# Optimization experiments

Hardware: AMD Instinct MI355X
Metric: run time of the kernel (lower is better)

Reference implementation:

```python
import jax, jax.numpy as jnp
import numpy as np

N, E, D, R = 50000, 1200000, 128, 6  # nodes, edges, channels (dim_in==dim_out), relations
NEG_SLOPE = 0.2


def setup_inputs() -> dict:
    key = jax.random.key(0)
    ks = jax.random.split(key, 7)
    x = jax.random.normal(ks[0], (N, D), jnp.float32)
    edge_index = jax.random.randint(ks[1], (2, E), 0, N)
    edge_type = jax.random.randint(ks[2], (E,), 0, R)
    # RGATConv params (heads=1): weight [R, D, D], q/k [D, 1], bias [D]
    weight = jax.random.normal(ks[3], (R, D, D), jnp.float32) * 0.05
    q = jax.random.normal(ks[4], (D, 1), jnp.float32) * 0.05
    k = jax.random.normal(ks[5], (D, 1), jnp.float32) * 0.05
    bias = jnp.zeros((D,), jnp.float32)
    return dict(x=x, edge_index=edge_index, edge_type=edge_type,
                weight=weight, q=q, k=k, bias=bias)


def segment_softmax(logits, seg, num_segments):
    m = jax.ops.segment_max(logits, seg, num_segments=num_segments)
    m = jnp.where(jnp.isfinite(m), m, 0.0)  # empty segments -> 0
    e = jnp.exp(logits - m[seg])
    s = jax.ops.segment_sum(e, seg, num_segments=num_segments)
    return e / (s[seg] + 1e-16)


def reference(x, edge_index, edge_type, weight, q, k, bias):
    src, dst = edge_index[0], edge_index[1]  # message flows src(j) -> dst(i)
    # per-node, per-relation transform W_r x_n : [R, N, D]
    hx = jnp.einsum('nd,rdo->rno', x, weight)
    # attention projections (heads=1): scalar per node per relation
    nq = jnp.einsum('rno,o->rn', hx, q[:, 0])  # q_i component
    nk = jnp.einsum('rno,o->rn', hx, k[:, 0])  # k_j component
    # additive self-attention, across-relation softmax over incoming edges
    logits = jax.nn.leaky_relu(nq[edge_type, dst] + nk[edge_type, src], NEG_SLOPE)
    alpha = segment_softmax(logits, dst, N)  # [E]
    # message = alpha * (W_r x_j), scatter-add into dst; dropout inactive (eval)
    msg = alpha[:, None] * hx[edge_type, src]  # [E, D]
    agg = jax.ops.segment_sum(msg, dst, num_segments=N) + bias
    out = agg + x  # residual add in GATLayer.forward
    return out, alpha[:, None]  # attention weights: [E, heads=1]
```

## Files before the change

kernel.cpp:

```cpp
#include <hip/hip_runtime.h>
#include <hip/hip_bf16.h>
#include <cstdint>

#define NN 50000
#define NE 1200000
#define DD 128
#define RR 6
#define NEG 0.2f
#define NB 391
#define CAP 4096
#define TILE 4096
#define GEMMB 782

typedef __hip_bfloat16 bf16;
typedef __attribute__((ext_vector_type(8))) short short8;
typedef __attribute__((ext_vector_type(4))) float f32x4;

__device__ __forceinline__ float bflo(unsigned u) { return __uint_as_float(u << 16); }
__device__ __forceinline__ float bfhi(unsigned u) { return __uint_as_float(u & 0xFFFF0000u); }
__device__ __forceinline__ ushort f2b(float v) {
  unsigned b = __float_as_uint(v);
  return (ushort)((b + 0x7FFFu + ((b >> 16) & 1u)) >> 16);
}

__global__ __launch_bounds__(256) void k_prep(const float* __restrict__ W,
    const float* __restrict__ qv, const float* __restrict__ kv,
    ushort* __restrict__ wp, ushort* __restrict__ wp7, int* __restrict__ bcur) {
  int t = blockIdx.x * 256 + threadIdx.x;
  if (t < NB) bcur[t] = 0;
  if (t < RR * 8 * 4 * 64) {
    int lane = t & 63;
    int ks = (t >> 6) & 3;
    int cf = (t >> 8) & 7;
    int r = t >> 11;
    int col = cf * 16 + (lane & 15);
    int k0 = ks * 32 + (lane >> 4) * 8;
    ushort* dst = wp + (size_t)t * 8;
    #pragma unroll
    for (int e = 0; e < 8; ++e)
      dst[e] = f2b(W[((size_t)r * DD + (k0 + e)) * DD + col]);
  } else if (t < RR * 8 * 4 * 64 + 256) {
    int idx = t - RR * 8 * 4 * 64;
    int lane = idx & 63, ks = idx >> 6;
    int col = lane & 15;
    int k0 = ks * 32 + (lane >> 4) * 8;
    ushort* dst = wp7 + (size_t)idx * 8;
    #pragma unroll
    for (int e = 0; e < 8; ++e) {
      float v = 0.f;
      if (col < 12) {
        int r = col < 6 ? col : col - 6;
        const float* vv = col < 6 ? qv : kv;
        const float* row = W + ((size_t)r * DD + (k0 + e)) * DD;
        for (int o = 0; o < DD; ++o) v += row[o] * vv[o];
      }
      dst[e] = f2b(v);
    }
  }
}

__global__ __launch_bounds__(256) void k_gemm(const float* __restrict__ x,
    const ushort* __restrict__ wp, const ushort* __restrict__ wp7,
    ushort* __restrict__ hx, float* __restrict__ nq, float* __restrict__ nk) {
  __shared__ ushort tile[64][136];
  int tid = threadIdx.x;
  int w = tid >> 6, l = tid & 63;
  int wrow = w & 1, wcol = w >> 1;
  int row0 = blockIdx.x * 64;
  int rbase = row0 + wrow * 32;
  int lr = l & 15, lg = l >> 4;

  short8 af[2][4];
  #pragma unroll
  for (int rf = 0; rf < 2; ++rf) {
    int row = rbase + rf * 16 + lr;
    row = row < NN ? row : NN - 1;
    const float* src = x + (size_t)row * DD + lg * 8;
    #pragma unroll
    for (int ks = 0; ks < 4; ++ks) {
      float4 u0 = *reinterpret_cast<const float4*>(src + ks * 32);
      float4 u1 = *reinterpret_cast<const float4*>(src + ks * 32 + 4);
      short8 a;
      a[0] = (short)f2b(u0.x); a[1] = (short)f2b(u0.y);
      a[2] = (short)f2b(u0.z); a[3] = (short)f2b(u0.w);
      a[4] = (short)f2b(u1.x); a[5] = (short)f2b(u1.y);
      a[6] = (short)f2b(u1.z); a[7] = (short)f2b(u1.w);
      af[rf][ks] = a;
    }
  }

  if (wcol == 0) {
    f32x4 aq0 = {0.f, 0.f, 0.f, 0.f}, aq1 = {0.f, 0.f, 0.f, 0.f};
    #pragma unroll
    for (int ks = 0; ks < 4; ++ks) {
      short8 b = *reinterpret_cast<const short8*>(wp7 + (size_t)(ks * 64 + l) * 8);
      aq0 = __builtin_amdgcn_mfma_f32_16x16x32_bf16(af[0][ks], b, aq0, 0, 0, 0);
      aq1 = __builtin_amdgcn_mfma_f32_16x16x32_bf16(af[1][ks], b, aq1, 0, 0, 0);
    }
    if (lr < 12) {
      float* pl = (lr < 6 ? nq + (size_t)lr * NN : nk + (size_t)(lr - 6) * NN);
      #pragma unroll
      for (int rf = 0; rf < 2; ++rf) {
        int rowb = rbase + rf * 16 + lg * 4;
        f32x4 v = rf ? aq1 : aq0;
        if (rowb + 3 < NN) {
          float4 o4 = make_float4(v[0], v[1], v[2], v[3]);
          *reinterpret_cast<float4*>(pl + rowb) = o4;
        } else {
          #pragma unroll
          for (int j = 0; j < 4; ++j) if (rowb + j < NN) pl[rowb + j] = v[j];
        }
      }
    }
  }

  for (int r = 0; r < RR; ++r) {
    #pragma unroll
    for (int cfl = 0; cfl < 4; ++cfl) {
      int cfg = wcol * 4 + cfl;
      const ushort* bp = wp + (((size_t)(r * 8 + cfg) * 4) * 64 + l) * 8;
      short8 b0 = *reinterpret_cast<const short8*>(bp);
      short8 b1 = *reinterpret_cast<const short8*>(bp + 512);
      short8 b2 = *reinterpret_cast<const short8*>(bp + 1024);
      short8 b3 = *reinterpret_cast<const short8*>(bp + 1536);
      f32x4 acc0 = {0.f, 0.f, 0.f, 0.f};
      f32x4 acc1 = {0.f, 0.f, 0.f, 0.f};
      acc0 = __builtin_amdgcn_mfma_f32_16x16x32_bf16(af[0][0], b0, acc0, 0, 0, 0);
      acc1 = __builtin_amdgcn_mfma_f32_16x16x32_bf16(af[1][0], b0, acc1, 0, 0, 0);
      acc0 = __builtin_amdgcn_mfma_f32_16x16x32_bf16(af[0][1], b1, acc0, 0, 0, 0);
      acc1 = __builtin_amdgcn_mfma_f32_16x16x32_bf16(af[1][1], b1, acc1, 0, 0, 0);
      acc0 = __builtin_amdgcn_mfma_f32_16x16x32_bf16(af[0][2], b2, acc0, 0, 0, 0);
      acc1 = __builtin_amdgcn_mfma_f32_16x16x32_bf16(af[1][2], b2, acc1, 0, 0, 0);
      acc0 = __builtin_amdgcn_mfma_f32_16x16x32_bf16(af[0][3], b3, acc0, 0, 0, 0);
      acc1 = __builtin_amdgcn_mfma_f32_16x16x32_bf16(af[1][3], b3, acc1, 0, 0, 0);

      int col = cfg * 16 + lr;
      #pragma unroll
      for (int rf = 0; rf < 2; ++rf) {
        int rowrel = wrow * 32 + rf * 16 + lg * 4;
        f32x4 ac = rf ? acc1 : acc0;
        #pragma unroll
        for (int j = 0; j < 4; ++j)
          tile[rowrel + j][col] = f2b(ac[j]);
      }
    }
    __syncthreads();
    #pragma unroll
    for (int it = 0; it < 4; ++it) {
      int rowrel = (tid >> 4) + it * 16;
      int grow = row0 + rowrel;
      uint4 v = *reinterpret_cast<const uint4*>(&tile[rowrel][(tid & 15) * 8]);
      if (grow < NN)
        *reinterpret_cast<uint4*>(hx + ((size_t)r * NN + grow) * DD + (tid & 15) * 8) = v;
    }
    __syncthreads();
  }
}

__global__ __launch_bounds__(256) void k_bscatter(const int* __restrict__ ei,
    const int* __restrict__ et, int* __restrict__ bcur,
    unsigned* __restrict__ bedge) {
  __shared__ unsigned sval[TILE];
  __shared__ unsigned short sbkt[TILE];
  __shared__ int lh[NB], lbase[NB], lcur[NB];
  int tid = threadIdx.x;
  int e0 = blockIdx.x * TILE;
  int lim = NE - e0; if (lim > TILE) lim = TILE;
  for (int i = tid; i < NB; i += 256) lh[i] = 0;
  __syncthreads();
  for (int i = tid; i < lim; i += 256) {
    int e = e0 + i;
    int s = ei[e], d = ei[NE + e], r = et[e];
    unsigned rowid = (unsigned)(r * NN + s);
    sval[i] = (rowid << 3) | (unsigned)r | ((unsigned)(d & 127) << 22);
    sbkt[i] = (unsigned short)(d >> 7);
    atomicAdd(&lh[d >> 7], 1);
  }
  __syncthreads();
  for (int i = tid; i < NB; i += 256) {
    int c = lh[i];
    lbase[i] = c ? atomicAdd(&bcur[i], c) : 0;
    lcur[i] = 0;
  }
  __syncthreads();
  for (int i = tid; i < lim; i += 256) {
    int b = sbkt[i];
    int pos = b * CAP + lbase[b] + atomicAdd(&lcur[b], 1);
    bedge[pos] = sval[i];
  }
}

__global__ __launch_bounds__(256) void k_bfinal(const unsigned* __restrict__ bedge,
    const int* __restrict__ bcur,
    const float* __restrict__ nq, const float* __restrict__ nk,
    int* __restrict__ deg, int* __restrict__ offs, unsigned* __restrict__ rec) {
  __shared__ int lh[128], sc_s[128], lcur[128];
  int b = blockIdx.x, tid = threadIdx.x;
  int base = b * CAP, cnt = bcur[b];
  if (tid < 128) lh[tid] = 0;
  __syncthreads();
  for (int i = tid; i < cnt; i += 256)
    atomicAdd(&lh[(bedge[base + i] >> 22) & 127], 1);
  __syncthreads();
  int v = 0;
  if (tid < 128) { v = lh[tid]; sc_s[tid] = v; }
  __syncthreads();
  for (int off = 1; off < 128; off <<= 1) {
    int u = (tid < 128 && tid >= off) ? sc_s[tid - off] : 0;
    __syncthreads();
    if (tid < 128) sc_s[tid] += u;
    __syncthreads();
  }
  if (tid < 128) {
    int excl = sc_s[tid] - v;
    int n = (b << 7) + tid;
    if (n < NN) { deg[n] = v; offs[n] = base + excl; }
    lcur[tid] = base + excl;
  }
  __syncthreads();
  for (int i = tid; i < cnt; i += 256) {
    unsigned be = bedge[base + i];
    unsigned rowid = (be >> 3) & 0x7FFFFu;
    int r = (int)(be & 7u);
    int dloc = (int)((be >> 22) & 127u);
    float l = nq[(size_t)r * NN + (b << 7) + dloc] + nk[rowid];
    l = l > 0.f ? l : NEG * l;
    float p = __expf(l);
    unsigned pb = (__float_as_uint(p) + 0x20000u) >> 18;
    int pos = atomicAdd(&lcur[dloc], 1);
    rec[pos] = (rowid << 13) | (pb & 0x1FFFu);
  }
}

__global__ __launch_bounds__(256) void k_agg(const float* __restrict__ x,
    const float* __restrict__ bias, const int* __restrict__ offs,
    const int* __restrict__ deg, const unsigned* __restrict__ rec,
    const bf16* __restrict__ hx, float* __restrict__ out,
    float* __restrict__ irec) {
  int g = threadIdx.x >> 5, lane = threadIdx.x & 31;
  int n = blockIdx.x * 8 + g;
  if (n >= NN) return;
  int base = offs[n], cnt = deg[n];
  const char* hp = (const char*)hx;
  int lo8 = lane * 8;

  float ssum = 0.f;
  float a0 = 0.f, a1 = 0.f, a2 = 0.f, a3 = 0.f;

#define DEC(E, OFF, P) unsigned OFF = ((E) >> 5) & 0xFFFFFF00u; \
                       float P = __uint_as_float(((E) & 0x1FFFu) << 18);

  int j = 0;
  for (; j + 7 < cnt; j += 8) {
    unsigned e0 = rec[base + j],     e1 = rec[base + j + 1];
    unsigned e2 = rec[base + j + 2], e3 = rec[base + j + 3];
    unsigned e4 = rec[base + j + 4], e5 = rec[base + j + 5];
    unsigned e6 = rec[base + j + 6], e7 = rec[base + j + 7];
    DEC(e0, o0, p0) DEC(e1, o1, p1) DEC(e2, o2, p2) DEC(e3, o3, p3)
    DEC(e4, o4, p4) DEC(e5, o5, p5) DEC(e6, o6, p6) DEC(e7, o7, p7)
    uint2 q0 = *reinterpret_cast<const uint2*>(hp + o0 + lo8);
    uint2 q1 = *reinterpret_cast<const uint2*>(hp + o1 + lo8);
    uint2 q2 = *reinterpret_cast<const uint2*>(hp + o2 + lo8);
    uint2 q3 = *reinterpret_cast<const uint2*>(hp + o3 + lo8);
    uint2 q4 = *reinterpret_cast<const uint2*>(hp + o4 + lo8);
    uint2 q5 = *reinterpret_cast<const uint2*>(hp + o5 + lo8);
    uint2 q6 = *reinterpret_cast<const uint2*>(hp + o6 + lo8);
    uint2 q7 = *reinterpret_cast<const uint2*>(hp + o7 + lo8);
    ssum += ((p0 + p1) + (p2 + p3)) + ((p4 + p5) + (p6 + p7));
    a0 += p0 * bflo(q0.x) + p1 * bflo(q1.x) + p2 * bflo(q2.x) + p3 * bflo(q3.x)
        + p4 * bflo(q4.x) + p5 * bflo(q5.x) + p6 * bflo(q6.x) + p7 * bflo(q7.x);
    a1 += p0 * bfhi(q0.x) + p1 * bfhi(q1.x) + p2 * bfhi(q2.x) + p3 * bfhi(q3.x)
        + p4 * bfhi(q4.x) + p5 * bfhi(q5.x) + p6 * bfhi(q6.x) + p7 * bfhi(q7.x);
    a2 += p0 * bflo(q0.y) + p1 * bflo(q1.y) + p2 * bflo(q2.y) + p3 * bflo(q3.y)
        + p4 * bflo(q4.y) + p5 * bflo(q5.y) + p6 * bflo(q6.y) + p7 * bflo(q7.y);
    a3 += p0 * bfhi(q0.y) + p1 * bfhi(q1.y) + p2 * bfhi(q2.y) + p3 * bfhi(q3.y)
        + p4 * bfhi(q4.y) + p5 * bfhi(q5.y) + p6 * bfhi(q6.y) + p7 * bfhi(q7.y);
  }
  for (; j + 3 < cnt; j += 4) {
    unsigned e0 = rec[base + j],     e1 = rec[base + j + 1];
    unsigned e2 = rec[base + j + 2], e3 = rec[base + j + 3];
    DEC(e0, o0, p0) DEC(e1, o1, p1) DEC(e2, o2, p2) DEC(e3, o3, p3)
    uint2 q0 = *reinterpret_cast<const uint2*>(hp + o0 + lo8);
    uint2 q1 = *reinterpret_cast<const uint2*>(hp + o1 + lo8);
    uint2 q2 = *reinterpret_cast<const uint2*>(hp + o2 + lo8);
    uint2 q3 = *reinterpret_cast<const uint2*>(hp + o3 + lo8);
    ssum += (p0 + p1) + (p2 + p3);
    a0 += p0 * bflo(q0.x) + p1 * bflo(q1.x) + p2 * bflo(q2.x) + p3 * bflo(q3.x);
    a1 += p0 * bfhi(q0.x) + p1 * bfhi(q1.x) + p2 * bfhi(q2.x) + p3 * bfhi(q3.x);
    a2 += p0 * bflo(q0.y) + p1 * bflo(q1.y) + p2 * bflo(q2.y) + p3 * bflo(q3.y);
    a3 += p0 * bfhi(q0.y) + p1 * bfhi(q1.y) + p2 * bfhi(q2.y) + p3 * bfhi(q3.y);
  }
  for (; j < cnt; ++j) {
    unsigned e0 = rec[base + j];
    DEC(e0, o0, p0)
    uint2 q0 = *reinterpret_cast<const uint2*>(hp + o0 + lo8);
    ssum += p0;
    a0 += p0 * bflo(q0.x);
    a1 += p0 * bfhi(q0.x);
    a2 += p0 * bflo(q0.y);
    a3 += p0 * bfhi(q0.y);
  }
#undef DEC

  float inv = 1.f / (ssum + 1e-16f);
  size_t o = (size_t)n * DD + lane * 4;
  float4 xb = *reinterpret_cast<const float4*>(x + o);
  float4 bb = *reinterpret_cast<const float4*>(bias + lane * 4);
  float4 res;
  res.x = xb.x + bb.x + a0 * inv;
  res.y = xb.y + bb.y + a1 * inv;
  res.z = xb.z + bb.z + a2 * inv;
  res.w = xb.w + bb.w + a3 * inv;
  *reinterpret_cast<float4*>(out + o) = res;

  if (lane == 0) irec[n] = inv;
}

__global__ __launch_bounds__(256) void k_alpha(const int* __restrict__ ei,
    const int* __restrict__ et, const float* __restrict__ nq,
    const float* __restrict__ nk, const float* __restrict__ irec,
    float* __restrict__ alpha) {
  int e = (blockIdx.x * 256 + threadIdx.x) * 2;
  if (e >= NE) return;
  int2 ss = *reinterpret_cast<const int2*>(ei + e);
  int2 dd = *reinterpret_cast<const int2*>(ei + NE + e);
  int2 rr = *reinterpret_cast<const int2*>(et + e);
  float l0 = nq[(size_t)rr.x * NN + dd.x] + nk[(size_t)rr.x * NN + ss.x];
  float l1 = nq[(size_t)rr.y * NN + dd.y] + nk[(size_t)rr.y * NN + ss.y];
  l0 = l0 > 0.f ? l0 : NEG * l0;
  l1 = l1 > 0.f ? l1 : NEG * l1;
  float2 res;
  res.x = __expf(l0) * irec[dd.x];
  res.y = __expf(l1) * irec[dd.y];
  *reinterpret_cast<float2*>(alpha + e) = res;
}

extern "C" void kernel_launch(void* const* d_in, const int* in_sizes, int n_in,
                              void* d_out, int out_size, void* d_ws, size_t ws_size,
                              hipStream_t stream) {
  const float* x    = (const float*)d_in[0];
  const int*   ei   = (const int*)d_in[1];
  const int*   et   = (const int*)d_in[2];
  const float* W    = (const float*)d_in[3];
  const float* qv   = (const float*)d_in[4];
  const float* kv   = (const float*)d_in[5];
  const float* bias = (const float*)d_in[6];

  float* out   = (float*)d_out;
  float* alpha = out + (size_t)NN * DD;

  char* p = (char*)d_ws;
  bf16*  hx      = (bf16*)p;    p += (size_t)RR * NN * DD * sizeof(bf16);
  float* nq      = (float*)p;   p += (size_t)RR * NN * sizeof(float);
  float* nk      = (float*)p;   p += (size_t)RR * NN * sizeof(float);
  int*   deg     = (int*)p;     p += NN * sizeof(int);
  int*   offs    = (int*)p;     p += NN * sizeof(int);
  float* irec    = (float*)p;   p += NN * sizeof(float);
  int*   bcur    = (int*)p;     p += NB * sizeof(int);
  p = (char*)(((uintptr_t)p + 15) & ~(uintptr_t)15);
  unsigned* bedge = (unsigned*)p; p += (size_t)NB * CAP * sizeof(unsigned);
  unsigned* rec  = (unsigned*)p;  p += (size_t)NB * CAP * sizeof(unsigned);
  ushort* wp     = (ushort*)p;  p += (size_t)RR * 8 * 4 * 64 * 8 * sizeof(ushort);
  ushort* wp7    = (ushort*)p;  p += (size_t)4 * 64 * 8 * sizeof(ushort);

  k_prep<<<49, 256, 0, stream>>>(W, qv, kv, wp, wp7, bcur);
  k_gemm<<<GEMMB, 256, 0, stream>>>(x, wp, wp7, (ushort*)hx, nq, nk);
  k_bscatter<<<(NE + TILE - 1) / TILE, 256, 0, stream>>>(ei, et, bcur, bedge);
  k_bfinal<<<NB, 256, 0, stream>>>(bedge, bcur, nq, nk, deg, offs, rec);
  k_agg<<<(NN + 7) / 8, 256, 0, stream>>>(x, bias, offs, deg, rec, hx, out, irec);
  k_alpha<<<(NE / 2 + 255) / 256, 256, 0, stream>>>(ei, et, nq, nk, irec, alpha);
}
```

Baseline: 177.3 us.

## Fuse GEMM and edge bucket-scatter into one launch with block-range dispatch

Merges the per-relation transform GEMM and the edge bucketing scatter into a single kernel. Blocks beyond the GEMM range do the scatter work, and the two paths share one shared-memory union. The two independent stages can then overlap on the device, and one kernel launch and its inter-kernel gap go away. The cost is that the shared-memory footprint becomes the larger of the two, about 25 KB for the scatter path, which may lower occupancy for the GEMM blocks.

```diff
diff --git a/kernel.cpp b/kernel.cpp
--- a/kernel.cpp
+++ b/kernel.cpp
@@ -11,6 +11,7 @@
 #define CAP 4096
 #define TILE 4096
 #define GEMMB 782
+#define SCB ((NE + TILE - 1) / TILE)
 
 typedef __hip_bfloat16 bf16;
 typedef __attribute__((ext_vector_type(8))) short short8;
@@ -59,11 +60,52 @@
   }
 }
 
-__global__ __launch_bounds__(256) void k_gemm(const float* __restrict__ x,
+union FSMem {
+  ushort tile[64][136];
+  struct {
+    unsigned sval[TILE];
+    unsigned short sbkt[TILE];
+    int lh[NB], lbase[NB], lcur[NB];
+  } c;
+};
+
+__global__ __launch_bounds__(256) void k_fused(const float* __restrict__ x,
     const ushort* __restrict__ wp, const ushort* __restrict__ wp7,
+    const int* __restrict__ ei, const int* __restrict__ et,
+    int* __restrict__ bcur, unsigned* __restrict__ bedge,
     ushort* __restrict__ hx, float* __restrict__ nq, float* __restrict__ nk) {
-  __shared__ ushort tile[64][136];
+  __shared__ FSMem sm;
   int tid = threadIdx.x;
+
+  if (blockIdx.x >= GEMMB) {
+    int blk = blockIdx.x - GEMMB;
+    int e0 = blk * TILE;
+    int lim = NE - e0; if (lim > TILE) lim = TILE;
+    for (int i = tid; i < NB; i += 256) sm.c.lh[i] = 0;
+    __syncthreads();
+    for (int i = tid; i < lim; i += 256) {
+      int e = e0 + i;
+      int s = ei[e], d = ei[NE + e], r = et[e];
+      unsigned rowid = (unsigned)(r * NN + s);
+      sm.c.sval[i] = (rowid << 3) | (unsigned)r | ((unsigned)(d & 127) << 22);
+      sm.c.sbkt[i] = (unsigned short)(d >> 7);
+      atomicAdd(&sm.c.lh[d >> 7], 1);
+    }
+    __syncthreads();
+    for (int i = tid; i < NB; i += 256) {
+      int c = sm.c.lh[i];
+      sm.c.lbase[i] = c ? atomicAdd(&bcur[i], c) : 0;
+      sm.c.lcur[i] = 0;
+    }
+    __syncthreads();
+    for (int i = tid; i < lim; i += 256) {
+      int b = sm.c.sbkt[i];
+      int pos = b * CAP + sm.c.lbase[b] + atomicAdd(&sm.c.lcur[b], 1);
+      bedge[pos] = sm.c.sval[i];
+    }
+    return;
+  }
+
   int w = tid >> 6, l = tid & 63;
   int wrow = w & 1, wcol = w >> 1;
   int row0 = blockIdx.x * 64;
@@ -141,7 +183,7 @@
         f32x4 ac = rf ? acc1 : acc0;
         #pragma unroll
         for (int j = 0; j < 4; ++j)
-          tile[rowrel + j][col] = f2b(ac[j]);
+          sm.tile[rowrel + j][col] = f2b(ac[j]);
       }
     }
     __syncthreads();
@@ -149,44 +191,11 @@
     for (int it = 0; it < 4; ++it) {
       int rowrel = (tid >> 4) + it * 16;
       int grow = row0 + rowrel;
-      uint4 v = *reinterpret_cast<const uint4*>(&tile[rowrel][(tid & 15) * 8]);
+      uint4 v = *reinterpret_cast<const uint4*>(&sm.tile[rowrel][(tid & 15) * 8]);
       if (grow < NN)
         *reinterpret_cast<uint4*>(hx + ((size_t)r * NN + grow) * DD + (tid & 15) * 8) = v;
     }
     __syncthreads();
-  }
-}
-
-__global__ __launch_bounds__(256) void k_bscatter(const int* __restrict__ ei,
-    const int* __restrict__ et, int* __restrict__ bcur,
-    unsigned* __restrict__ bedge) {
-  __shared__ unsigned sval[TILE];
-  __shared__ unsigned short sbkt[TILE];
-  __shared__ int lh[NB], lbase[NB], lcur[NB];
-  int tid = threadIdx.x;
-  int e0 = blockIdx.x * TILE;
-  int lim = NE - e0; if (lim > TILE) lim = TILE;
-  for (int i = tid; i < NB; i += 256) lh[i] = 0;
-  __syncthreads();
-  for (int i = tid; i < lim; i += 256) {
-    int e = e0 + i;
-    int s = ei[e], d = ei[NE + e], r = et[e];
-    unsigned rowid = (unsigned)(r * NN + s);
-    sval[i] = (rowid << 3) | (unsigned)r | ((unsigned)(d & 127) << 22);
-    sbkt[i] = (unsigned short)(d >> 7);
-    atomicAdd(&lh[d >> 7], 1);
-  }
-  __syncthreads();
-  for (int i = tid; i < NB; i += 256) {
-    int c = lh[i];
-    lbase[i] = c ? atomicAdd(&bcur[i], c) : 0;
-    lcur[i] = 0;
-  }
-  __syncthreads();
-  for (int i = tid; i < lim; i += 256) {
-    int b = sbkt[i];
-    int pos = b * CAP + lbase[b] + atomicAdd(&lcur[b], 1);
-    bedge[pos] = sval[i];
   }
 }
 
@@ -364,8 +373,8 @@
   ushort* wp7    = (ushort*)p;  p += (size_t)4 * 64 * 8 * sizeof(ushort);
 
   k_prep<<<49, 256, 0, stream>>>(W, qv, kv, wp, wp7, bcur);
-  k_gemm<<<GEMMB, 256, 0, stream>>>(x, wp, wp7, (ushort*)hx, nq, nk);
-  k_bscatter<<<(NE + TILE - 1) / TILE, 256, 0, stream>>>(ei, et, bcur, bedge);
+  k_fused<<<GEMMB + SCB, 256, 0, stream>>>(x, wp, wp7, ei, et, bcur, bedge,
+                                           (ushort*)hx, nq, nk);
   k_bfinal<<<NB, 256, 0, stream>>>(bedge, bcur, nq, nk, deg, offs, rec);
   k_agg<<<(NN + 7) / 8, 256, 0, stream>>>(x, bias, offs, deg, rec, hx, out, irec);
   k_alpha<<<(NE / 2 + 255) / 256, 256, 0, stream>>>(ei, et, nq, nk, irec, alpha);
```

New measurement: 161.7 us (median of 2 runs). 1.1x faster.
